# Performance work log

Measured on AMD Instinct MI355X. Metric: run time of the kernel, lower is better.

## Reference

```python
import jax, jax.numpy as jnp
import numpy as np

N = 100000
E = 3200000
D = 128
EPS = 1e-5


def setup_inputs() -> dict:
    key = jax.random.key(0)
    ks = jax.random.split(key, 9)
    h = jax.random.normal(ks[0], (N, D), dtype=jnp.float32)
    src = jax.random.randint(ks[1], (E,), 0, N, dtype=jnp.int64)
    dst = jax.random.randint(ks[2], (E,), 0, N, dtype=jnp.int64)
    s = 1.0 / np.sqrt(D)
    W_self = jax.random.uniform(ks[3], (D, D), jnp.float32, -s, s)
    W_neigh = jax.random.uniform(ks[4], (D, D), jnp.float32, -s, s)
    b = jax.random.uniform(ks[5], (D,), jnp.float32, -s, s)
    gamma = jnp.ones((D,), jnp.float32)
    beta = jnp.zeros((D,), jnp.float32)
    return {"h": h, "src": src, "dst": dst, "W_self": W_self,
            "W_neigh": W_neigh, "b": b, "gamma": gamma, "beta": beta}


def reference(h, src, dst, W_self, W_neigh, b, gamma, beta):
    # --- SAGEConv, mean aggregator (dropout p=0 -> identity) ---
    # gather source features along edges, segment-mean into destination nodes
    neigh_sum = jax.ops.segment_sum(h[src], dst, num_segments=N)      # [N, D]
    deg = jax.ops.segment_sum(jnp.ones((E,), h.dtype), dst, num_segments=N)
    neigh = neigh_sum / jnp.maximum(deg, 1.0)[:, None]                # [N, D]
    rst = h @ W_self + neigh @ W_neigh + b                            # [N, D]
    rst = jax.nn.relu(rst)                                            # activation
    # --- BatchNorm1d (training-mode batch statistics) ---
    mean = jnp.mean(rst, axis=0)
    var = jnp.var(rst, axis=0)
    rst = (rst - mean) * jax.lax.rsqrt(var + EPS) * gamma + beta
    # --- residual (in_feats == out_feats) ---
    return h + rst
```

## Files before the change

### kernel.cpp

```cpp
#include <hip/hip_runtime.h>

#define DCAP 2432
#define NBMAX 1600
#define SCATB 256
#define CONV2 512
#define WPB2 32
#define GB 1024
#define EORDCAP 3456

typedef __attribute__((ext_vector_type(2))) float f32x2;
typedef __attribute__((ext_vector_type(4))) float f32x4;
typedef __attribute__((ext_vector_type(8))) short bf16x8;

__device__ __forceinline__ unsigned short f2bf(float f) {
  union { float f; unsigned u; } c; c.f = f;
  unsigned u = c.u;
  unsigned r = u + 0x7FFFu + ((u >> 16) & 1u);
  return (unsigned short)(r >> 16);
}
__device__ __forceinline__ float bf2f(unsigned short s) {
  union { unsigned u; float f; } c; c.u = ((unsigned)s) << 16;
  return c.f;
}

__global__ __launch_bounds__(1024) void k_prescat(const float* __restrict__ h,
                                                  unsigned short* __restrict__ X,
                                                  unsigned* __restrict__ X8,
                                                  const float* __restrict__ Ws,
                                                  const float* __restrict__ Wn,
                                                  unsigned short* __restrict__ Wt,
                                                  const int* __restrict__ dst,
                                                  const int* __restrict__ src,
                                                  unsigned* __restrict__ esort,
                                                  int* __restrict__ gcur,
                                                  int nnodes, int E, int NB, int chunk) {
  __shared__ int cnt[NBMAX];
  __shared__ int gbase[NBMAX];
  int t = threadIdx.x;
  int bid = blockIdx.x;
  if (bid < SCATB) {
    int e0 = bid * chunk;
    int e1 = e0 + chunk; if (e1 > E) e1 = E;
    int n = e1 - e0;
    for (int i = t; i < NB; i += 1024) cnt[i] = 0;
    __syncthreads();
    for (int i = t; i < n; i += 1024)
      atomicAdd(&cnt[dst[e0 + i] >> 6], 1);
    __syncthreads();
    for (int bb = t; bb < NB; bb += 1024) {
      int len = cnt[bb];
      gbase[bb] = len ? atomicAdd(&gcur[bb], len) : 0;
      cnt[bb] = 0;
    }
    __syncthreads();
    for (int i = t; i < n; i += 1024) {
      int d = dst[e0 + i];
      int bb = d >> 6;
      int pos = gbase[bb] + atomicAdd(&cnt[bb], 1);
      if (pos < DCAP)
        esort[(long)bb * DCAP + pos] = ((unsigned)src[e0 + i] << 6) | (unsigned)(d & 63);
    }
  } else if (bid < SCATB + CONV2) {
    int stride = CONV2 * 1024;
    int total = nnodes * 32;
    for (int i = (bid - SCATB) * 1024 + t; i < total; i += stride) {
      int n = i >> 5, c = i & 31;
      float4 v = *(const float4*)(h + (long)n * 128 + c * 4);
      ushort4 o;
      o.x = f2bf(v.x); o.y = f2bf(v.y); o.z = f2bf(v.z); o.w = f2bf(v.w);
      *(ushort4*)(X + (long)n * 256 + c * 4) = o;
      int p8 = __builtin_amdgcn_cvt_pk_fp8_f32(v.x, v.y, 0, false);
      p8 = __builtin_amdgcn_cvt_pk_fp8_f32(v.z, v.w, p8, true);
      X8[(long)n * 32 + c] = (unsigned)p8;
    }
  } else if (bid < SCATB + CONV2 + WPB2) {
    int i = (bid - SCATB - CONV2) * 1024 + t;
    int col = i >> 8, k = i & 255;
    float v = (k < 128) ? Ws[k * 128 + col] : Wn[(k - 128) * 128 + col];
    Wt[col * 256 + k] = f2bf(v);
  } else {
    if (t < 32) X8[(long)nnodes * 32 + t] = 0u;
  }
}

__global__ __launch_bounds__(256) void k_aggb(unsigned short* __restrict__ X,
                                              const unsigned char* __restrict__ X8,
                                              const unsigned* __restrict__ esort,
                                              const int* __restrict__ gcur,
                                              int nnodes) {
  __shared__ unsigned eord[EORDCAP];
  __shared__ int dcnt[64], dstart[64], dcur[64], sc[64];
  int t = threadIdx.x;
  int b = blockIdx.x;
  int cntE = gcur[b]; if (cntE > DCAP) cntE = DCAP;
  const unsigned* ep = esort + (long)b * DCAP;
  if (t < 64) dcnt[t] = 0;
  __syncthreads();
  for (int i = t; i < cntE; i += 256)
    atomicAdd(&dcnt[ep[i] & 63u], 1);
  __syncthreads();
  int plen_t = 0;
  if (t < 64) { plen_t = (dcnt[t] + 15) & ~15; sc[t] = plen_t; }
  __syncthreads();
  for (int off = 1; off < 64; off <<= 1) {
    int v = (t < 64 && t >= off) ? sc[t - off] : 0;
    __syncthreads();
    if (t < 64) sc[t] += v;
    __syncthreads();
  }
  if (t < 64) { int ex = sc[t] - plen_t; dstart[t] = ex; dcur[t] = ex; }
  __syncthreads();
  int tot = sc[63];
  for (int i = t; i < tot; i += 256) eord[i] = (unsigned)nnodes;
  __syncthreads();
  for (int i = t; i < cntE; i += 256) {
    unsigned e = ep[i];
    int pos = atomicAdd(&dcur[e & 63u], 1);
    eord[pos] = e >> 6;
  }
  __syncthreads();

  int lane = t & 63, w = t >> 6;
  int qt = lane >> 4, ql = lane & 15;
  int ndst = nnodes - b * 64; if (ndst > 64) ndst = 64;
  for (int dl = w; dl < ndst; dl += 4) {
    int start = dstart[dl], dn = dcnt[dl];
    int plen = (dn + 15) & ~15;
    f32x2 acc[2][4];
#pragma unroll
    for (int u = 0; u < 2; u++)
#pragma unroll
      for (int j = 0; j < 4; j++) { acc[u][j].x = 0.f; acc[u][j].y = 0.f; }
    int i = 0;
    for (; i + 32 <= plen; i += 32) {
      uint2 v[8];
#pragma unroll
      for (int u = 0; u < 8; u++) {
        unsigned e = eord[start + i + u * 4 + qt];
        v[u] = *(const uint2*)(X8 + e * 128u + ql * 8u);
      }
#pragma unroll
      for (int u = 0; u < 8; u++) {
        acc[u & 1][0] += __builtin_amdgcn_cvt_pk_f32_fp8(v[u].x, false);
        acc[u & 1][1] += __builtin_amdgcn_cvt_pk_f32_fp8(v[u].x, true);
        acc[u & 1][2] += __builtin_amdgcn_cvt_pk_f32_fp8(v[u].y, false);
        acc[u & 1][3] += __builtin_amdgcn_cvt_pk_f32_fp8(v[u].y, true);
      }
    }
    if (i < plen) {
      uint2 v[4];
#pragma unroll
      for (int u = 0; u < 4; u++) {
        unsigned e = eord[start + i + u * 4 + qt];
        v[u] = *(const uint2*)(X8 + e * 128u + ql * 8u);
      }
#pragma unroll
      for (int u = 0; u < 4; u++) {
        acc[u & 1][0] += __builtin_amdgcn_cvt_pk_f32_fp8(v[u].x, false);
        acc[u & 1][1] += __builtin_amdgcn_cvt_pk_f32_fp8(v[u].x, true);
        acc[u & 1][2] += __builtin_amdgcn_cvt_pk_f32_fp8(v[u].y, false);
        acc[u & 1][3] += __builtin_amdgcn_cvt_pk_f32_fp8(v[u].y, true);
      }
    }
    float s[8];
#pragma unroll
    for (int j = 0; j < 4; j++) {
      s[2 * j] = acc[0][j].x + acc[1][j].x;
      s[2 * j + 1] = acc[0][j].y + acc[1][j].y;
    }
#pragma unroll
    for (int j = 0; j < 8; j++) {
      s[j] += __shfl_down(s[j], 32);
      s[j] += __shfl_down(s[j], 16);
    }
    if (qt == 0) {
      float scl = 1.0f / fmaxf((float)dn, 1.0f);
      uint4 o;
      o.x = (unsigned)f2bf(s[0] * scl) | ((unsigned)f2bf(s[1] * scl) << 16);
      o.y = (unsigned)f2bf(s[2] * scl) | ((unsigned)f2bf(s[3] * scl) << 16);
      o.z = (unsigned)f2bf(s[4] * scl) | ((unsigned)f2bf(s[5] * scl) << 16);
      o.w = (unsigned)f2bf(s[6] * scl) | ((unsigned)f2bf(s[7] * scl) << 16);
      *(uint4*)(X + (long)(b * 64 + dl) * 256 + 128 + ql * 8) = o;
    }
  }
}

__global__ __launch_bounds__(256) void k_gemm(const unsigned short* __restrict__ X,
                                              const unsigned short* __restrict__ Wt,
                                              const float* __restrict__ bias,
                                              unsigned short* __restrict__ rst8,
                                              float* __restrict__ psumA,
                                              float* __restrict__ psqA,
                                              int nnodes, int ntiles) {
  __shared__ unsigned short atile[2][16][256];
  int t = threadIdx.x;
  int w = t >> 6, lane = t & 63;
  int m = lane & 15, q = lane >> 4;
  int col0 = w * 32 + m;
  int col1 = col0 + 16;
  bf16x8 b0[8], b1[8];
#pragma unroll
  for (int ks = 0; ks < 8; ks++) {
    b0[ks] = *(const bf16x8*)(Wt + col0 * 256 + q * 8 + ks * 32);
    b1[ks] = *(const bf16x8*)(Wt + col1 * 256 + q * 8 + ks * 32);
  }
  float bv0 = bias[col0], bv1 = bias[col1];
  float s0 = 0.f, sq0 = 0.f, s1 = 0.f, sq1 = 0.f;

#define STAGE(bufi, tb_)                                                        \
  {                                                                             \
    int r_ = t >> 4;                                                            \
    long row_ = (long)(tb_) * 16 + r_;                                          \
    if (row_ >= nnodes) row_ = nnodes - 1;                                      \
    const unsigned short* gp_ = X + row_ * 256 + (t & 15) * 16;                 \
    uint4 d0_ = *(const uint4*)gp_;                                             \
    uint4 d1_ = *(const uint4*)(gp_ + 8);                                       \
    int bo_ = (t & 15) * 32;                                                    \
    char* lb_ = (char*)&atile[bufi][0][0] + r_ * 512;                           \
    *(uint4*)(lb_ + (bo_ ^ ((r_ & 7) << 4))) = d0_;                             \
    *(uint4*)(lb_ + ((bo_ + 16) ^ ((r_ & 7) << 4))) = d1_;                      \
  }

  int tb = blockIdx.x;
  int it = 0;
  if (tb < ntiles) STAGE(0, tb);
  for (; tb < ntiles; tb += GB, ++it) {
    __syncthreads();
    const char* lb = (const char*)&atile[it & 1][0][0] + m * 512;
    bf16x8 a[8];
#pragma unroll
    for (int ks = 0; ks < 8; ks++)
      a[ks] = *(const bf16x8*)(lb + ((q * 16 + ks * 64) ^ ((m & 7) << 4)));
    int tbn = tb + GB;
    if (tbn < ntiles) STAGE((it + 1) & 1, tbn);
    f32x4 acc0 = {0.f, 0.f, 0.f, 0.f};
    f32x4 acc1 = {0.f, 0.f, 0.f, 0.f};
#pragma unroll
    for (int ks = 0; ks < 8; ks++) {
      acc0 = __builtin_amdgcn_mfma_f32_16x16x32_bf16(a[ks], b0[ks], acc0, 0, 0, 0);
      acc1 = __builtin_amdgcn_mfma_f32_16x16x32_bf16(a[ks], b1[ks], acc1, 0, 0, 0);
    }
#pragma unroll
    for (int r = 0; r < 4; r++) {
      int row = tb * 16 + q * 4 + r;
      if (row < nnodes) {
        float v0 = acc0[r] + bv0; v0 = v0 > 0.f ? v0 : 0.f;
        float v1 = acc1[r] + bv1; v1 = v1 > 0.f ? v1 : 0.f;
        rst8[(long)row * 128 + col0] = f2bf(v0);
        rst8[(long)row * 128 + col1] = f2bf(v1);
        s0 += v0; sq0 += v0 * v0;
        s1 += v1; sq1 += v1 * v1;
      }
    }
  }
#undef STAGE

  s0 += __shfl_down(s0, 32);  s0 += __shfl_down(s0, 16);
  sq0 += __shfl_down(sq0, 32); sq0 += __shfl_down(sq0, 16);
  s1 += __shfl_down(s1, 32);  s1 += __shfl_down(s1, 16);
  sq1 += __shfl_down(sq1, 32); sq1 += __shfl_down(sq1, 16);
  if (lane < 16) {
    atomicAdd(&psumA[col0], s0);
    atomicAdd(&psumA[col1], s1);
    atomicAdd(&psqA[col0], sq0);
    atomicAdd(&psqA[col1], sq1);
  }
}

__global__ void k_final(const unsigned short* __restrict__ X,
                        float* __restrict__ out,
                        const unsigned short* __restrict__ rst8,
                        const float* __restrict__ psumA,
                        const float* __restrict__ psqA,
                        const float* __restrict__ gamma,
                        const float* __restrict__ beta,
                        int nnodes, float Nf) {
  __shared__ float sc_s[128], sh_s[128];
  int t = threadIdx.x;
  if (t < 128) {
    float s = psumA[t], s2 = psqA[t];
    float mean = s / Nf;
    float var = s2 / Nf - mean * mean;
    float inv = rsqrtf(var + 1e-5f);
    float scv = gamma[t] * inv;
    sc_s[t] = scv;
    sh_s[t] = beta[t] - mean * scv;
  }
  __syncthreads();
  long stride = (long)gridDim.x * blockDim.x;
  long total = (long)nnodes * 16;
  for (long i = (long)blockIdx.x * blockDim.x + t; i < total; i += stride) {
    int c = (int)(i & 15);
    long row = i >> 4;
    uint4 rv = *(const uint4*)(rst8 + i * 8);
    uint4 hv = *(const uint4*)(X + row * 256 + c * 8);
    float4 sc0 = *(const float4*)(sc_s + c * 8);
    float4 sc1 = *(const float4*)(sc_s + c * 8 + 4);
    float4 sh0 = *(const float4*)(sh_s + c * 8);
    float4 sh1 = *(const float4*)(sh_s + c * 8 + 4);
    float4 o0, o1;
    o0.x = bf2f((unsigned short)(hv.x & 0xFFFFu)) + bf2f((unsigned short)(rv.x & 0xFFFFu)) * sc0.x + sh0.x;
    o0.y = bf2f((unsigned short)(hv.x >> 16))     + bf2f((unsigned short)(rv.x >> 16)) * sc0.y + sh0.y;
    o0.z = bf2f((unsigned short)(hv.y & 0xFFFFu)) + bf2f((unsigned short)(rv.y & 0xFFFFu)) * sc0.z + sh0.z;
    o0.w = bf2f((unsigned short)(hv.y >> 16))     + bf2f((unsigned short)(rv.y >> 16)) * sc0.w + sh0.w;
    o1.x = bf2f((unsigned short)(hv.z & 0xFFFFu)) + bf2f((unsigned short)(rv.z & 0xFFFFu)) * sc1.x + sh1.x;
    o1.y = bf2f((unsigned short)(hv.z >> 16))     + bf2f((unsigned short)(rv.z >> 16)) * sc1.y + sh1.y;
    o1.z = bf2f((unsigned short)(hv.w & 0xFFFFu)) + bf2f((unsigned short)(rv.w & 0xFFFFu)) * sc1.z + sh1.z;
    o1.w = bf2f((unsigned short)(hv.w >> 16))     + bf2f((unsigned short)(rv.w >> 16)) * sc1.w + sh1.w;
    *(float4*)(out + i * 8) = o0;
    *(float4*)(out + i * 8 + 4) = o1;
  }
}

extern "C" void kernel_launch(void* const* d_in, const int* in_sizes, int n_in,
                              void* d_out, int out_size, void* d_ws, size_t ws_size,
                              hipStream_t stream) {
  const float* h     = (const float*)d_in[0];
  const int*   src   = (const int*)d_in[1];
  const int*   dst   = (const int*)d_in[2];
  const float* Ws    = (const float*)d_in[3];
  const float* Wn    = (const float*)d_in[4];
  const float* bias  = (const float*)d_in[5];
  const float* gamma = (const float*)d_in[6];
  const float* beta  = (const float*)d_in[7];
  float* out = (float*)d_out;

  int nnodes = in_sizes[0] / 128;
  int E = in_sizes[1];
  int NB = (nnodes + 63) >> 6;
  int ntiles = (nnodes + 15) >> 4;
  int chunk = (E + SCATB - 1) / SCATB;

  char* ws = (char*)d_ws;
  size_t off = 0;
  unsigned short* X = (unsigned short*)(ws + off); off += (size_t)nnodes * 256 * 2;
  size_t off_alias = off;
  unsigned* X8 = (unsigned*)(ws + off);            off += (size_t)(nnodes + 1) * 128;
  unsigned* esort = (unsigned*)(ws + off);         off += (size_t)NB * DCAP * 4;
  unsigned short* rst8 = (unsigned short*)(ws + off_alias);
  unsigned short* Wt = (unsigned short*)(ws + off); off += 128 * 256 * 2;
  int* gcur = (int*)(ws + off);                    off += (size_t)NBMAX * 4;
  float* psumA = (float*)(ws + off);               off += 512;
  float* psqA = (float*)(ws + off);                off += 512;

  hipMemsetAsync(gcur, 0, (size_t)NBMAX * 4 + 1024, stream);
  k_prescat<<<SCATB + CONV2 + WPB2 + 1, 1024, 0, stream>>>(
      h, X, X8, Ws, Wn, Wt, dst, src, esort, gcur, nnodes, E, NB, chunk);
  k_aggb<<<NB, 256, 0, stream>>>(X, (const unsigned char*)X8, esort, gcur, nnodes);
  k_gemm<<<GB, 256, 0, stream>>>(X, Wt, bias, rst8, psumA, psqA, nnodes, ntiles);
  k_final<<<4096, 256, 0, stream>>>(X, out, rst8, psumA, psqA, gamma, beta,
                                    nnodes, (float)nnodes);
}
```

Measured before the change: 290.6 us.

## Fuse dense GEMM into aggregation kernel and pad per-bucket atomic counters

Removes the separate GEMM kernel. Each aggregation block now runs the MFMA GEMM for its own 64 nodes right after computing their neighbour means, and writes the ReLU output back into the neighbour half of X in place. That drops a launch and a grid-wide pass over X, though it lowers GEMM occupancy and adds per-block reloads of the weights. The per-bucket global atomic counters are also spaced 16 ints apart to avoid false sharing on the cache lines they share. The in-place overwrite of X's neighbour half relies on a block-level barrier placed between each row tile's loads and its stores.

```diff
diff --git a/kernel.cpp b/kernel.cpp
--- a/kernel.cpp
+++ b/kernel.cpp
@@ -5,8 +5,8 @@
 #define SCATB 256
 #define CONV2 512
 #define WPB2 32
-#define GB 1024
 #define EORDCAP 3456
+#define GPAD 16
 
 typedef __attribute__((ext_vector_type(2))) float f32x2;
 typedef __attribute__((ext_vector_type(4))) float f32x4;
@@ -49,7 +49,7 @@
     __syncthreads();
     for (int bb = t; bb < NB; bb += 1024) {
       int len = cnt[bb];
-      gbase[bb] = len ? atomicAdd(&gcur[bb], len) : 0;
+      gbase[bb] = len ? atomicAdd(&gcur[bb * GPAD], len) : 0;
       cnt[bb] = 0;
     }
     __syncthreads();
@@ -87,12 +87,16 @@
                                               const unsigned char* __restrict__ X8,
                                               const unsigned* __restrict__ esort,
                                               const int* __restrict__ gcur,
+                                              const unsigned short* __restrict__ Wt,
+                                              const float* __restrict__ bias,
+                                              float* __restrict__ psumA,
+                                              float* __restrict__ psqA,
                                               int nnodes) {
   __shared__ unsigned eord[EORDCAP];
   __shared__ int dcnt[64], dstart[64], dcur[64], sc[64];
   int t = threadIdx.x;
   int b = blockIdx.x;
-  int cntE = gcur[b]; if (cntE > DCAP) cntE = DCAP;
+  int cntE = gcur[b * GPAD]; if (cntE > DCAP) cntE = DCAP;
   const unsigned* ep = esort + (long)b * DCAP;
   if (t < 64) dcnt[t] = 0;
   __syncthreads();
@@ -183,93 +187,64 @@
       *(uint4*)(X + (long)(b * 64 + dl) * 256 + 128 + ql * 8) = o;
     }
   }
-}
-
-__global__ __launch_bounds__(256) void k_gemm(const unsigned short* __restrict__ X,
-                                              const unsigned short* __restrict__ Wt,
-                                              const float* __restrict__ bias,
-                                              unsigned short* __restrict__ rst8,
-                                              float* __restrict__ psumA,
-                                              float* __restrict__ psqA,
-                                              int nnodes, int ntiles) {
-  __shared__ unsigned short atile[2][16][256];
-  int t = threadIdx.x;
-  int w = t >> 6, lane = t & 63;
-  int m = lane & 15, q = lane >> 4;
-  int col0 = w * 32 + m;
-  int col1 = col0 + 16;
-  bf16x8 b0[8], b1[8];
-#pragma unroll
-  for (int ks = 0; ks < 8; ks++) {
-    b0[ks] = *(const bf16x8*)(Wt + col0 * 256 + q * 8 + ks * 32);
-    b1[ks] = *(const bf16x8*)(Wt + col1 * 256 + q * 8 + ks * 32);
-  }
-  float bv0 = bias[col0], bv1 = bias[col1];
-  float s0 = 0.f, sq0 = 0.f, s1 = 0.f, sq1 = 0.f;
-
-#define STAGE(bufi, tb_)                                                        \
-  {                                                                             \
-    int r_ = t >> 4;                                                            \
-    long row_ = (long)(tb_) * 16 + r_;                                          \
-    if (row_ >= nnodes) row_ = nnodes - 1;                                      \
-    const unsigned short* gp_ = X + row_ * 256 + (t & 15) * 16;                 \
-    uint4 d0_ = *(const uint4*)gp_;                                             \
-    uint4 d1_ = *(const uint4*)(gp_ + 8);                                       \
-    int bo_ = (t & 15) * 32;                                                    \
-    char* lb_ = (char*)&atile[bufi][0][0] + r_ * 512;                           \
-    *(uint4*)(lb_ + (bo_ ^ ((r_ & 7) << 4))) = d0_;                             \
-    *(uint4*)(lb_ + ((bo_ + 16) ^ ((r_ & 7) << 4))) = d1_;                      \
-  }
-
-  int tb = blockIdx.x;
-  int it = 0;
-  if (tb < ntiles) STAGE(0, tb);
-  for (; tb < ntiles; tb += GB, ++it) {
-    __syncthreads();
-    const char* lb = (const char*)&atile[it & 1][0][0] + m * 512;
-    bf16x8 a[8];
-#pragma unroll
-    for (int ks = 0; ks < 8; ks++)
-      a[ks] = *(const bf16x8*)(lb + ((q * 16 + ks * 64) ^ ((m & 7) << 4)));
-    int tbn = tb + GB;
-    if (tbn < ntiles) STAGE((it + 1) & 1, tbn);
-    f32x4 acc0 = {0.f, 0.f, 0.f, 0.f};
-    f32x4 acc1 = {0.f, 0.f, 0.f, 0.f};
+
+  __syncthreads();
+  {
+    int m2 = lane & 15, q2 = lane >> 4;
+    int col0 = w * 32 + m2;
+    int col1 = col0 + 16;
+    bf16x8 b0[8], b1[8];
 #pragma unroll
     for (int ks = 0; ks < 8; ks++) {
-      acc0 = __builtin_amdgcn_mfma_f32_16x16x32_bf16(a[ks], b0[ks], acc0, 0, 0, 0);
-      acc1 = __builtin_amdgcn_mfma_f32_16x16x32_bf16(a[ks], b1[ks], acc1, 0, 0, 0);
-    }
-#pragma unroll
-    for (int r = 0; r < 4; r++) {
-      int row = tb * 16 + q * 4 + r;
-      if (row < nnodes) {
-        float v0 = acc0[r] + bv0; v0 = v0 > 0.f ? v0 : 0.f;
-        float v1 = acc1[r] + bv1; v1 = v1 > 0.f ? v1 : 0.f;
-        rst8[(long)row * 128 + col0] = f2bf(v0);
-        rst8[(long)row * 128 + col1] = f2bf(v1);
-        s0 += v0; sq0 += v0 * v0;
-        s1 += v1; sq1 += v1 * v1;
-      }
-    }
-  }
-#undef STAGE
-
-  s0 += __shfl_down(s0, 32);  s0 += __shfl_down(s0, 16);
-  sq0 += __shfl_down(sq0, 32); sq0 += __shfl_down(sq0, 16);
-  s1 += __shfl_down(s1, 32);  s1 += __shfl_down(s1, 16);
-  sq1 += __shfl_down(sq1, 32); sq1 += __shfl_down(sq1, 16);
-  if (lane < 16) {
-    atomicAdd(&psumA[col0], s0);
-    atomicAdd(&psumA[col1], s1);
-    atomicAdd(&psqA[col0], sq0);
-    atomicAdd(&psqA[col1], sq1);
+      b0[ks] = *(const bf16x8*)(Wt + col0 * 256 + q2 * 8 + ks * 32);
+      b1[ks] = *(const bf16x8*)(Wt + col1 * 256 + q2 * 8 + ks * 32);
+    }
+    float bv0 = bias[col0], bv1 = bias[col1];
+    float s0 = 0.f, sq0 = 0.f, s1 = 0.f, sq1 = 0.f;
+#pragma unroll
+    for (int rt = 0; rt < 4; ++rt) {
+      int rowm = b * 64 + rt * 16 + m2;
+      if (rowm >= nnodes) rowm = nnodes - 1;
+      const unsigned short* xp = X + (long)rowm * 256 + q2 * 8;
+      bf16x8 a[8];
+#pragma unroll
+      for (int ks = 0; ks < 8; ks++) a[ks] = *(const bf16x8*)(xp + ks * 32);
+      __syncthreads();
+      f32x4 acc0 = {0.f, 0.f, 0.f, 0.f};
+      f32x4 acc1 = {0.f, 0.f, 0.f, 0.f};
+#pragma unroll
+      for (int ks = 0; ks < 8; ks++) {
+        acc0 = __builtin_amdgcn_mfma_f32_16x16x32_bf16(a[ks], b0[ks], acc0, 0, 0, 0);
+        acc1 = __builtin_amdgcn_mfma_f32_16x16x32_bf16(a[ks], b1[ks], acc1, 0, 0, 0);
+      }
+#pragma unroll
+      for (int r = 0; r < 4; r++) {
+        int row = b * 64 + rt * 16 + q2 * 4 + r;
+        if (row < nnodes) {
+          float v0 = acc0[r] + bv0; v0 = v0 > 0.f ? v0 : 0.f;
+          float v1 = acc1[r] + bv1; v1 = v1 > 0.f ? v1 : 0.f;
+          X[(long)row * 256 + 128 + col0] = f2bf(v0);
+          X[(long)row * 256 + 128 + col1] = f2bf(v1);
+          s0 += v0; sq0 += v0 * v0;
+          s1 += v1; sq1 += v1 * v1;
+        }
+      }
+    }
+    s0 += __shfl_down(s0, 32);  s0 += __shfl_down(s0, 16);
+    sq0 += __shfl_down(sq0, 32); sq0 += __shfl_down(sq0, 16);
+    s1 += __shfl_down(s1, 32);  s1 += __shfl_down(s1, 16);
+    sq1 += __shfl_down(sq1, 32); sq1 += __shfl_down(sq1, 16);
+    if (lane < 16) {
+      atomicAdd(&psumA[col0], s0);
+      atomicAdd(&psumA[col1], s1);
+      atomicAdd(&psqA[col0], sq0);
+      atomicAdd(&psqA[col1], sq1);
+    }
   }
 }
 
 __global__ void k_final(const unsigned short* __restrict__ X,
                         float* __restrict__ out,
-                        const unsigned short* __restrict__ rst8,
                         const float* __restrict__ psumA,
                         const float* __restrict__ psqA,
                         const float* __restrict__ gamma,
@@ -292,8 +267,8 @@
   for (long i = (long)blockIdx.x * blockDim.x + t; i < total; i += stride) {
     int c = (int)(i & 15);
     long row = i >> 4;
-    uint4 rv = *(const uint4*)(rst8 + i * 8);
     uint4 hv = *(const uint4*)(X + row * 256 + c * 8);
+    uint4 rv = *(const uint4*)(X + row * 256 + 128 + c * 8);
     float4 sc0 = *(const float4*)(sc_s + c * 8);
     float4 sc1 = *(const float4*)(sc_s + c * 8 + 4);
     float4 sh0 = *(const float4*)(sh_s + c * 8);
@@ -328,26 +303,23 @@
   int nnodes = in_sizes[0] / 128;
   int E = in_sizes[1];
   int NB = (nnodes + 63) >> 6;
-  int ntiles = (nnodes + 15) >> 4;
   int chunk = (E + SCATB - 1) / SCATB;
 
   char* ws = (char*)d_ws;
   size_t off = 0;
   unsigned short* X = (unsigned short*)(ws + off); off += (size_t)nnodes * 256 * 2;
-  size_t off_alias = off;
   unsigned* X8 = (unsigned*)(ws + off);            off += (size_t)(nnodes + 1) * 128;
   unsigned* esort = (unsigned*)(ws + off);         off += (size_t)NB * DCAP * 4;
-  unsigned short* rst8 = (unsigned short*)(ws + off_alias);
   unsigned short* Wt = (unsigned short*)(ws + off); off += 128 * 256 * 2;
-  int* gcur = (int*)(ws + off);                    off += (size_t)NBMAX * 4;
+  int* gcur = (int*)(ws + off);                    off += (size_t)NBMAX * GPAD * 4;
   float* psumA = (float*)(ws + off);               off += 512;
   float* psqA = (float*)(ws + off);                off += 512;
 
-  hipMemsetAsync(gcur, 0, (size_t)NBMAX * 4 + 1024, stream);
+  hipMemsetAsync(gcur, 0, (size_t)NBMAX * GPAD * 4 + 1024, stream);
   k_prescat<<<SCATB + CONV2 + WPB2 + 1, 1024, 0, stream>>>(
       h, X, X8, Ws, Wn, Wt, dst, src, esort, gcur, nnodes, E, NB, chunk);
-  k_aggb<<<NB, 256, 0, stream>>>(X, (const unsigned char*)X8, esort, gcur, nnodes);
-  k_gemm<<<GB, 256, 0, stream>>>(X, Wt, bias, rst8, psumA, psqA, nnodes, ntiles);
-  k_final<<<4096, 256, 0, stream>>>(X, out, rst8, psumA, psqA, gamma, beta,
+  k_aggb<<<NB, 256, 0, stream>>>(X, (const unsigned char*)X8, esort, gcur,
+                                 Wt, bias, psumA, psqA, nnodes);
+  k_final<<<4096, 256, 0, stream>>>(X, out, psumA, psqA, gamma, beta,
                                     nnodes, (float)nnodes);
 }
```

Result: slower. 316.6 us (+9.0%).
